# Kernel optimization log

Hardware: AMD Instinct MI355X
Metric: run time of the kernel (lower is better)

## Reference

```python
import jax, jax.numpy as jnp
import numpy as np

J_NUM = 24
# SMPL kinematic tree: parents[i] < i for all i >= 1 (root has parent -1)
PARENTS = np.array([-1, 0, 0, 0, 1, 2, 3, 4, 5, 6, 7, 8, 9, 9, 9, 12, 13, 14,
                    16, 17, 18, 19, 20, 21], dtype=np.int32)
BATCH = 131072


def setup_inputs() -> dict:
    key = jax.random.key(0)
    k1, k2, k3 = jax.random.split(key, 3)
    pose = jax.random.normal(k1, (BATCH, J_NUM, 3), dtype=jnp.float32) * 0.3
    trans = jax.random.normal(k2, (BATCH, 3), dtype=jnp.float32)
    # Rest-pose joint transforms: identity rotation + random local offset (learned buffer)
    offs = jax.random.normal(k3, (J_NUM, 3), dtype=jnp.float32) * 0.1
    J = jnp.tile(jnp.eye(4, dtype=jnp.float32)[None], (J_NUM, 1, 1))
    J = J.at[:, :3, 3].set(offs)
    parents = jnp.asarray(PARENTS, dtype=jnp.int32)
    return {"pose": pose, "trans": trans, "J": J, "parents": parents}


def rodrigues(r):
    """Axis-angle [..., 3] -> rotation matrices [..., 3, 3] (batched Rodrigues)."""
    theta = jnp.sqrt(jnp.sum(r * r, axis=-1, keepdims=True) + 1e-16)  # [...,1]
    rh = r / theta
    x, y, z = rh[..., 0], rh[..., 1], rh[..., 2]
    zero = jnp.zeros_like(x)
    K = jnp.stack([zero, -z, y, z, zero, -x, -y, x, zero], axis=-1)
    K = K.reshape(r.shape[:-1] + (3, 3))
    c = jnp.cos(theta)[..., None]
    s = jnp.sin(theta)[..., None]
    outer = rh[..., :, None] * rh[..., None, :]
    I3 = jnp.eye(3, dtype=r.dtype)
    return c * I3 + (1.0 - c) * outer + s * K


def reference(pose, trans, J, parents):
    par = np.asarray(parents)  # static tree structure
    B, Jn = pose.shape[0], pose.shape[1]
    R = rodrigues(pose)                                   # [B,J,3,3]
    # embed into 4x4 homogeneous transforms
    R4 = jnp.pad(R, ((0, 0), (0, 0), (0, 1), (0, 1)))
    R4 = R4.at[:, :, 3, 3].set(1.0)                       # [B,J,4,4]
    # local transform per joint: J[i] @ localRot[i] (batched once)
    local = jnp.einsum('jab,njbc->njac', J, R4)           # [B,J,4,4]
    # sequential kinematic-tree composition (fixed small unrolled loop)
    results = [local[:, 0]]
    for i in range(1, Jn):
        results.append(jnp.matmul(results[int(par[i])], local[:, i]))
    stacked = jnp.stack(results, axis=1)                  # [B,J,4,4]
    J_posed = stacked[:, :, :3, 3] + trans[:, None, :]    # [B,J,3]
    return J_posed
```

## Files before the change

### kernel.cpp

```cpp
#include <hip/hip_runtime.h>

#define J_NUM 24
#define BLOCK 64
#define PER_ELEM 72
#define LDS_FLOATS (BLOCK * PER_ELEM)

__global__ __launch_bounds__(BLOCK)
void fk_kernel(const float* __restrict__ pose, const float* __restrict__ trans,
               const float* __restrict__ Jm, float* __restrict__ out)
{
    __shared__ float s[LDS_FLOATS];

    const int t = threadIdx.x;
    const size_t blockBase = (size_t)blockIdx.x * BLOCK;
    const int b = (int)blockBase + t;

    {
        const float4* src = reinterpret_cast<const float4*>(pose + blockBase * PER_ELEM);
        float4* dst = reinterpret_cast<float4*>(s);
#pragma unroll
        for (int i = 0; i < 18; ++i)
            dst[i * BLOCK + t] = src[i * BLOCK + t];
    }
    __syncthreads();

    float* p = s + t * PER_ELEM;

    const float t0 = trans[(size_t)b * 3 + 0];
    const float t1 = trans[(size_t)b * 3 + 1];
    const float t2 = trans[(size_t)b * 3 + 2];

    const int par[J_NUM] = {-1,0,0,0,1,2,3,4,5,6,7,8,9,9,9,12,13,14,16,17,18,19,20,21};

    float Rc[J_NUM][9];
    float Pc[J_NUM][3];

#pragma unroll
    for (int j = 0; j < J_NUM; ++j) {
        float rx = p[j*3+0], ry = p[j*3+1], rz = p[j*3+2];
        float tt = rx*rx + ry*ry + rz*rz + 1e-16f;
        float inv = rsqrtf(tt);
        float theta = tt * inv;
        float x = rx*inv, y = ry*inv, z = rz*inv;
        float c = __cosf(theta), sn = __sinf(theta);
        float C = 1.0f - c;

        float R0 = c + C*x*x;
        float R1 = C*x*y - sn*z;
        float R2 = C*x*z + sn*y;
        float R3 = C*y*x + sn*z;
        float R4 = c + C*y*y;
        float R5 = C*y*z - sn*x;
        float R6 = C*z*x - sn*y;
        float R7 = C*z*y + sn*x;
        float R8 = c + C*z*z;

        float ox = Jm[j*16 + 3];
        float oy = Jm[j*16 + 7];
        float oz = Jm[j*16 + 11];

        if (j == 0) {
            Rc[0][0]=R0; Rc[0][1]=R1; Rc[0][2]=R2;
            Rc[0][3]=R3; Rc[0][4]=R4; Rc[0][5]=R5;
            Rc[0][6]=R6; Rc[0][7]=R7; Rc[0][8]=R8;
            Pc[0][0]=ox; Pc[0][1]=oy; Pc[0][2]=oz;
        } else {
            const int q = par[j];
            Pc[j][0] = Pc[q][0] + Rc[q][0]*ox + Rc[q][1]*oy + Rc[q][2]*oz;
            Pc[j][1] = Pc[q][1] + Rc[q][3]*ox + Rc[q][4]*oy + Rc[q][5]*oz;
            Pc[j][2] = Pc[q][2] + Rc[q][6]*ox + Rc[q][7]*oy + Rc[q][8]*oz;
            Rc[j][0] = Rc[q][0]*R0 + Rc[q][1]*R3 + Rc[q][2]*R6;
            Rc[j][1] = Rc[q][0]*R1 + Rc[q][1]*R4 + Rc[q][2]*R7;
            Rc[j][2] = Rc[q][0]*R2 + Rc[q][1]*R5 + Rc[q][2]*R8;
            Rc[j][3] = Rc[q][3]*R0 + Rc[q][4]*R3 + Rc[q][5]*R6;
            Rc[j][4] = Rc[q][3]*R1 + Rc[q][4]*R4 + Rc[q][5]*R7;
            Rc[j][5] = Rc[q][3]*R2 + Rc[q][4]*R5 + Rc[q][5]*R8;
            Rc[j][6] = Rc[q][6]*R0 + Rc[q][7]*R3 + Rc[q][8]*R6;
            Rc[j][7] = Rc[q][6]*R1 + Rc[q][7]*R4 + Rc[q][8]*R7;
            Rc[j][8] = Rc[q][6]*R2 + Rc[q][7]*R5 + Rc[q][8]*R8;
        }

        p[j*3+0] = Pc[j][0] + t0;
        p[j*3+1] = Pc[j][1] + t1;
        p[j*3+2] = Pc[j][2] + t2;
    }

    __syncthreads();

    {
        const float4* src = reinterpret_cast<const float4*>(s);
        float4* dst = reinterpret_cast<float4*>(out + blockBase * PER_ELEM);
#pragma unroll
        for (int i = 0; i < 18; ++i)
            dst[i * BLOCK + t] = src[i * BLOCK + t];
    }
}

extern "C" void kernel_launch(void* const* d_in, const int* in_sizes, int n_in,
                              void* d_out, int out_size, void* d_ws, size_t ws_size,
                              hipStream_t stream) {
    const float* pose  = (const float*)d_in[0];
    const float* trans = (const float*)d_in[1];
    const float* Jm    = (const float*)d_in[2];
    float* out = (float*)d_out;

    int B = in_sizes[0] / (J_NUM * 3);
    int blocks = B / BLOCK;
    fk_kernel<<<blocks, BLOCK, 0, stream>>>(pose, trans, Jm, out);
}
```

Measured before the change: 93.85 us.

## Split each batch element across three threads, one per rotation row

Each batch element is now handled by three threads, each owning one row of the accumulated rotation and one position component. This cuts per-thread register state from 24x12 to 24x4 floats, which should lift occupancy and spread the chain across more lanes. The LDS layout is padded to stride 73 to avoid bank conflicts on the strided per-element reads. In exchange, all three threads redundantly compute the full Rodrigues rotation for every joint, and there is an extra barrier plus scalar LDS stores before write-out.

```diff
diff --git a/kernel.cpp b/kernel.cpp
--- a/kernel.cpp
+++ b/kernel.cpp
@@ -1,98 +1,108 @@
 #include <hip/hip_runtime.h>
 
 #define J_NUM 24
-#define BLOCK 64
-#define PER_ELEM 72
-#define LDS_FLOATS (BLOCK * PER_ELEM)
+#define ELEMS 64
+#define NTHREADS (ELEMS * 3)
+#define STRIDE 73
 
-__global__ __launch_bounds__(BLOCK)
+__global__ __launch_bounds__(NTHREADS)
 void fk_kernel(const float* __restrict__ pose, const float* __restrict__ trans,
                const float* __restrict__ Jm, float* __restrict__ out)
 {
-    __shared__ float s[LDS_FLOATS];
+    __shared__ float s[ELEMS * STRIDE];
 
-    const int t = threadIdx.x;
-    const size_t blockBase = (size_t)blockIdx.x * BLOCK;
-    const int b = (int)blockBase + t;
+    const int u = threadIdx.x;
+    const size_t blockBase = (size_t)blockIdx.x * ELEMS;
 
     {
-        const float4* src = reinterpret_cast<const float4*>(pose + blockBase * PER_ELEM);
-        float4* dst = reinterpret_cast<float4*>(s);
+        const float4* src = reinterpret_cast<const float4*>(pose + blockBase * 72);
 #pragma unroll
-        for (int i = 0; i < 18; ++i)
-            dst[i * BLOCK + t] = src[i * BLOCK + t];
+        for (int i = 0; i < 6; ++i) {
+            int m = i * NTHREADS + u;
+            float4 v = src[m];
+            int e = m / 18;
+            int f = (m - e * 18) * 4;
+            float* d = s + e * STRIDE + f;
+            d[0] = v.x; d[1] = v.y; d[2] = v.z; d[3] = v.w;
+        }
     }
+
+    const float tr = trans[blockBase * 3 + u];
+
     __syncthreads();
 
-    float* p = s + t * PER_ELEM;
-
-    const float t0 = trans[(size_t)b * 3 + 0];
-    const float t1 = trans[(size_t)b * 3 + 1];
-    const float t2 = trans[(size_t)b * 3 + 2];
+    const int e = u / 3;
+    const int r = u - e * 3;
+    const float* p = s + e * STRIDE;
 
     const int par[J_NUM] = {-1,0,0,0,1,2,3,4,5,6,7,8,9,9,9,12,13,14,16,17,18,19,20,21};
 
-    float Rc[J_NUM][9];
-    float Pc[J_NUM][3];
+    float rcx[J_NUM], rcy[J_NUM], rcz[J_NUM];
+    float pc[J_NUM];
 
 #pragma unroll
     for (int j = 0; j < J_NUM; ++j) {
-        float rx = p[j*3+0], ry = p[j*3+1], rz = p[j*3+2];
-        float tt = rx*rx + ry*ry + rz*rz + 1e-16f;
+        float ax = p[j*3+0], ay = p[j*3+1], az = p[j*3+2];
+        float tt = ax*ax + ay*ay + az*az + 1e-16f;
         float inv = rsqrtf(tt);
-        float theta = tt * inv;
-        float x = rx*inv, y = ry*inv, z = rz*inv;
-        float c = __cosf(theta), sn = __sinf(theta);
+        float th = tt * inv;
+        float x = ax*inv, y = ay*inv, z = az*inv;
+        float c = __cosf(th), sn = __sinf(th);
         float C = 1.0f - c;
-
-        float R0 = c + C*x*x;
-        float R1 = C*x*y - sn*z;
-        float R2 = C*x*z + sn*y;
-        float R3 = C*y*x + sn*z;
-        float R4 = c + C*y*y;
-        float R5 = C*y*z - sn*x;
-        float R6 = C*z*x - sn*y;
-        float R7 = C*z*y + sn*x;
-        float R8 = c + C*z*z;
+        float cx = C*x, cy = C*y, cz = C*z;
+        float sx = sn*x, sy = sn*y, sz = sn*z;
+        float R0 = fmaf(cx, x, c);
+        float R1 = fmaf(cx, y, -sz);
+        float R2 = fmaf(cx, z,  sy);
+        float R3 = fmaf(cy, x,  sz);
+        float R4 = fmaf(cy, y, c);
+        float R5 = fmaf(cy, z, -sx);
+        float R6 = fmaf(cz, x, -sy);
+        float R7 = fmaf(cz, y,  sx);
+        float R8 = fmaf(cz, z, c);
 
         float ox = Jm[j*16 + 3];
         float oy = Jm[j*16 + 7];
         float oz = Jm[j*16 + 11];
 
         if (j == 0) {
-            Rc[0][0]=R0; Rc[0][1]=R1; Rc[0][2]=R2;
-            Rc[0][3]=R3; Rc[0][4]=R4; Rc[0][5]=R5;
-            Rc[0][6]=R6; Rc[0][7]=R7; Rc[0][8]=R8;
-            Pc[0][0]=ox; Pc[0][1]=oy; Pc[0][2]=oz;
+            rcx[0] = (r == 0) ? R0 : ((r == 1) ? R3 : R6);
+            rcy[0] = (r == 0) ? R1 : ((r == 1) ? R4 : R7);
+            rcz[0] = (r == 0) ? R2 : ((r == 1) ? R5 : R8);
+            pc[0]  = (r == 0) ? ox : ((r == 1) ? oy : oz);
         } else {
             const int q = par[j];
-            Pc[j][0] = Pc[q][0] + Rc[q][0]*ox + Rc[q][1]*oy + Rc[q][2]*oz;
-            Pc[j][1] = Pc[q][1] + Rc[q][3]*ox + Rc[q][4]*oy + Rc[q][5]*oz;
-            Pc[j][2] = Pc[q][2] + Rc[q][6]*ox + Rc[q][7]*oy + Rc[q][8]*oz;
-            Rc[j][0] = Rc[q][0]*R0 + Rc[q][1]*R3 + Rc[q][2]*R6;
-            Rc[j][1] = Rc[q][0]*R1 + Rc[q][1]*R4 + Rc[q][2]*R7;
-            Rc[j][2] = Rc[q][0]*R2 + Rc[q][1]*R5 + Rc[q][2]*R8;
-            Rc[j][3] = Rc[q][3]*R0 + Rc[q][4]*R3 + Rc[q][5]*R6;
-            Rc[j][4] = Rc[q][3]*R1 + Rc[q][4]*R4 + Rc[q][5]*R7;
-            Rc[j][5] = Rc[q][3]*R2 + Rc[q][4]*R5 + Rc[q][5]*R8;
-            Rc[j][6] = Rc[q][6]*R0 + Rc[q][7]*R3 + Rc[q][8]*R6;
-            Rc[j][7] = Rc[q][6]*R1 + Rc[q][7]*R4 + Rc[q][8]*R7;
-            Rc[j][8] = Rc[q][6]*R2 + Rc[q][7]*R5 + Rc[q][8]*R8;
+            float c0 = rcx[q], c1 = rcy[q], c2 = rcz[q];
+            pc[j]  = pc[q] + c0*ox + c1*oy + c2*oz;
+            rcx[j] = c0*R0 + c1*R3 + c2*R6;
+            rcy[j] = c0*R1 + c1*R4 + c2*R7;
+            rcz[j] = c0*R2 + c1*R5 + c2*R8;
         }
-
-        p[j*3+0] = Pc[j][0] + t0;
-        p[j*3+1] = Pc[j][1] + t1;
-        p[j*3+2] = Pc[j][2] + t2;
     }
 
     __syncthreads();
 
     {
-        const float4* src = reinterpret_cast<const float4*>(s);
-        float4* dst = reinterpret_cast<float4*>(out + blockBase * PER_ELEM);
+        float* w = s + e * STRIDE + r;
 #pragma unroll
-        for (int i = 0; i < 18; ++i)
-            dst[i * BLOCK + t] = src[i * BLOCK + t];
+        for (int j = 0; j < J_NUM; ++j)
+            w[j*3] = pc[j] + tr;
+    }
+
+    __syncthreads();
+
+    {
+        float4* dst = reinterpret_cast<float4*>(out + blockBase * 72);
+#pragma unroll
+        for (int i = 0; i < 6; ++i) {
+            int m = i * NTHREADS + u;
+            int e2 = m / 18;
+            int f = (m - e2 * 18) * 4;
+            const float* src = s + e2 * STRIDE + f;
+            float4 v;
+            v.x = src[0]; v.y = src[1]; v.z = src[2]; v.w = src[3];
+            dst[m] = v;
+        }
     }
 }
 
@@ -105,6 +115,6 @@
     float* out = (float*)d_out;
 
     int B = in_sizes[0] / (J_NUM * 3);
-    int blocks = B / BLOCK;
-    fk_kernel<<<blocks, BLOCK, 0, stream>>>(pose, trans, Jm, out);
+    int blocks = B / ELEMS;
+    fk_kernel<<<blocks, NTHREADS, 0, stream>>>(pose, trans, Jm, out);
 }
```

Result: slower. 96.13 us (+2.4%).
